# Kernel tuning notes

Measured on AMD Instinct MI355X. Metric: run time of the kernel, lower is better.

## Reference

```python
import jax, jax.numpy as jnp
import numpy as np

D_MODEL = 1024
N_HIDDEN = 64   # per-head dim (outer factor of packed proj dim)
N_HEAD = 16
B, L = 2, 2048


def setup_inputs() -> dict:
    key = jax.random.key(0)
    ks = jax.random.split(key, 7)
    s = 0.02
    return {
        "q": jax.random.normal(ks[0], (B, L, D_MODEL), dtype=jnp.float32),
        "k": jax.random.normal(ks[1], (B, L, D_MODEL), dtype=jnp.float32),
        "v": jax.random.normal(ks[2], (B, L, D_MODEL), dtype=jnp.float32),
        # torch nn.Linear weights: shape (out_features, in_features), y = x @ W.T
        "W_Q": jax.random.normal(ks[3], (N_HIDDEN * N_HEAD, D_MODEL), dtype=jnp.float32) * s,
        "W_K": jax.random.normal(ks[4], (N_HIDDEN * N_HEAD, D_MODEL), dtype=jnp.float32) * s,
        "W_V": jax.random.normal(ks[5], (N_HIDDEN * N_HEAD, D_MODEL), dtype=jnp.float32) * s,
        "W_O": jax.random.normal(ks[6], (D_MODEL, N_HEAD * N_HIDDEN), dtype=jnp.float32) * s,
    }


def reference(q, k, v, W_Q, W_K, W_V, W_O):
    b, l, _ = q.shape
    # projections (bias=False)
    qp = q @ W_Q.T  # [b,l,n_hidden*n_head]
    kp = k @ W_K.T
    vp = v @ W_V.T
    # rearrange 'b l (c h) -> b l c h' with c=n_hidden: hidden is OUTER factor
    qh = qp.reshape(b, l, N_HIDDEN, N_HEAD)
    kh = kp.reshape(b, l, N_HIDDEN, N_HEAD)
    vh = vp.reshape(b, l, N_HIDDEN, N_HEAD)
    scores = jnp.einsum('bldh,bjdh->bhlj', qh, kh) / np.float32(np.sqrt(N_HIDDEN))
    attn = jax.nn.softmax(scores, axis=-1)
    out = jnp.einsum('bhlj,bjdh->bldh', attn, vh)  # [b,l,n_hidden,n_head]
    out = out.reshape(b, l, N_HIDDEN * N_HEAD)      # 'b l d h -> b l (d h)'
    return out @ W_O.T
```

## Files before the change

### kernel.cpp

```cpp
#include <hip/hip_runtime.h>
#include <hip/hip_bf16.h>
#include <stdint.h>

typedef __attribute__((ext_vector_type(8))) short short8;
typedef __attribute__((ext_vector_type(4))) float f32x4;
typedef __attribute__((ext_vector_type(16))) float f32x16;
typedef __attribute__((ext_vector_type(2))) int int2v;
typedef unsigned short u16;
typedef unsigned int u32;


__device__ __forceinline__ u16 bf16rne(float f) {
  u32 u = __builtin_bit_cast(u32, f);
  u += 0x7FFFu + ((u >> 16) & 1u);
  return (u16)(u >> 16);
}

__device__ __forceinline__ u32 cvtpk(float lo, float hi) {
  u32 r;
  asm("v_cvt_pk_bf16_f32 %0, %1, %2" : "=v"(r) : "v"(lo), "v"(hi));
  return r;
}

__device__ __forceinline__ void gl_lds16(const u16* g, u16* l) {
  __builtin_amdgcn_global_load_lds((const __attribute__((address_space(1))) void*)g,
                                   (__attribute__((address_space(3))) void*)l, 16, 0, 0);
}

struct CastArgs {
  const float* src[7];
  u16* dst[7];
  int n4[7];
};

__global__ void cast_all(CastArgs a) {
  const int id = blockIdx.y;
  const float* __restrict__ s = a.src[id];
  u16* __restrict__ d = a.dst[id];
  const int stride = gridDim.x * blockDim.x;
  const int i0 = blockIdx.x * blockDim.x + threadIdx.x;
  if (id < 6) {
    const int n4 = a.n4[id];
    for (int i = i0; i < n4; i += stride) {
      float4 v = ((const float4*)s)[i];
      u32 lo = (u32)bf16rne(v.x) | ((u32)bf16rne(v.y) << 16);
      u32 hi = (u32)bf16rne(v.z) | ((u32)bf16rne(v.w) << 16);
      ((uint2*)d)[i] = make_uint2(lo, hi);
    }
  } else {
    const int n = a.n4[6];
    for (int i = i0; i < n; i += stride) {
      int row = i >> 10, c = i & 1023;
      int hh = c >> 6, dd = c & 63;
      d[i] = bf16rne(s[(row << 10) + dd * 16 + hh]);
    }
  }
}

template<int AHEADS>
__device__ __forceinline__ void gemm_body(const u16* __restrict__ A, const u16* __restrict__ Bw,
                                          void* __restrict__ Cd, int epi, float ascale) {
  const int bn = blockIdx.x * 128, bm = blockIdx.y * 128;
  const int tid = threadIdx.x, lane = tid & 63, w = tid >> 6;
  const int wr = w >> 1, wc = w & 1;
  __shared__ __align__(16) u16 As[128 * 64];
  __shared__ __align__(16) u16 Bs[128 * 64];
  f32x4 acc[4][4];
#pragma unroll
  for (int m = 0; m < 4; ++m)
#pragma unroll
    for (int n = 0; n < 4; ++n) acc[m][n] = (f32x4){0.f, 0.f, 0.f, 0.f};

  for (int kt = 0; kt < 16; ++kt) {
#pragma unroll
    for (int i = 0; i < 4; ++i) {
      int c = tid + i * 256;
      int row = c >> 3, kc = c & 7;
      int swz = (kc ^ (row & 7)) << 3;
      const u16* srcA;
      if (AHEADS) {
        int bA = bm >> 11;
        int lrow = (bm & 2047) + row;
        srcA = A + ((size_t)(bA * 16 + kt) * 2048 + lrow) * 64 + swz;
      } else {
        srcA = A + (size_t)(bm + row) * 1024 + kt * 64 + swz;
      }
      gl_lds16(srcA, &As[c * 8]);
      const u16* srcB = Bw + (size_t)(bn + row) * 1024 + kt * 64 + swz;
      gl_lds16(srcB, &Bs[c * 8]);
    }
    __syncthreads();
#pragma unroll
    for (int ks = 0; ks < 2; ++ks) {
      const int ck = ks * 4 + (lane >> 4);
      short8 af[4], bfr[4];
#pragma unroll
      for (int m = 0; m < 4; ++m) {
        int r = wr * 64 + m * 16 + (lane & 15);
        af[m] = *(const short8*)&As[(r * 8 + (ck ^ (r & 7))) * 8];
      }
#pragma unroll
      for (int n = 0; n < 4; ++n) {
        int r = wc * 64 + n * 16 + (lane & 15);
        bfr[n] = *(const short8*)&Bs[(r * 8 + (ck ^ (r & 7))) * 8];
      }
#pragma unroll
      for (int m = 0; m < 4; ++m)
#pragma unroll
        for (int n = 0; n < 4; ++n)
          acc[m][n] = __builtin_amdgcn_mfma_f32_16x16x32_bf16(af[m], bfr[n], acc[m][n], 0, 0, 0);
    }
    __syncthreads();
  }

  const int lrow4 = (lane >> 4) << 2;
  const int h = lane & 15;
  if (epi == 0) {
    u16* D = (u16*)Cd;
    const int dbase = (bn + wc * 64) >> 4;
#pragma unroll
    for (int m = 0; m < 4; ++m)
#pragma unroll
      for (int i = 0; i < 4; ++i) {
        int R = bm + wr * 64 + m * 16 + lrow4 + i;
        int b = R >> 11, l = R & 2047;
        u32 lo = (u32)bf16rne(acc[m][0][i] * ascale) | ((u32)bf16rne(acc[m][1][i] * ascale) << 16);
        u32 hi = (u32)bf16rne(acc[m][2][i] * ascale) | ((u32)bf16rne(acc[m][3][i] * ascale) << 16);
        size_t addr = ((size_t)((b * 16 + h) * 2048 + l)) * 64 + dbase;
        *(uint2*)(D + addr) = make_uint2(lo, hi);
      }
  } else if (epi == 1) {
    u16* D = (u16*)Cd;
    const int dbase = (bn + wc * 64) >> 4;
    const int b = bm >> 11;
#pragma unroll
    for (int m = 0; m < 4; ++m) {
      int l0 = (bm & 2047) + wr * 64 + m * 16 + lrow4;
#pragma unroll
      for (int n = 0; n < 4; ++n) {
        int d = dbase + n;
        u32 lo = (u32)bf16rne(acc[m][n][0]) | ((u32)bf16rne(acc[m][n][1]) << 16);
        u32 hi = (u32)bf16rne(acc[m][n][2]) | ((u32)bf16rne(acc[m][n][3]) << 16);
        size_t addr = ((size_t)((b * 16 + h) * 64 + d)) * 2048 + l0;
        *(uint2*)(D + addr) = make_uint2(lo, hi);
      }
    }
  } else {
    float* D = (float*)Cd;
#pragma unroll
    for (int m = 0; m < 4; ++m)
#pragma unroll
      for (int i = 0; i < 4; ++i) {
        int R = bm + wr * 64 + m * 16 + lrow4 + i;
        size_t base = (size_t)R * 1024 + bn + wc * 64 + (lane & 15);
#pragma unroll
        for (int n = 0; n < 4; ++n) D[base + n * 16] = acc[m][n][i];
      }
  }
}

struct ProjArgs { const u16* A[3]; const u16* W[3]; u16* D[3]; float scale[3]; };

__global__ __launch_bounds__(256, 2) void gemm_proj(ProjArgs pa) {
  const int z = blockIdx.z;
  gemm_body<0>(pa.A[z], pa.W[z], pa.D[z], z == 2 ? 1 : 0, pa.scale[z]);
}

__global__ __launch_bounds__(256, 2) void gemm_oproj(const u16* __restrict__ A,
                                                     const u16* __restrict__ W,
                                                     float* __restrict__ C) {
  gemm_body<1>(A, W, C, 2, 1.0f);
}

__global__ __launch_bounds__(128, 2) void attn_kernel(const u16* __restrict__ Qh,
                                                      const u16* __restrict__ Kh,
                                                      const u16* __restrict__ Vt,
                                                      u16* __restrict__ Oh) {
  const int hb = blockIdx.x;
  const int qt = blockIdx.y;
  const int tid = threadIdx.x, lane = tid & 63, w = tid >> 6;
  const int l31 = lane & 31, hi = lane >> 5;
  __shared__ __align__(16) u16 Ks[2][64 * 64];
  __shared__ __align__(16) u16 Vs[2][64 * 64];

  const u16* Qg = Qh + (size_t)hb * (2048 * 64);
  const u16* Kg = Kh + (size_t)hb * (2048 * 64);
  const u16* Vg = Vt + (size_t)hb * (64 * 2048);
  const int qrow = qt * 64 + w * 32 + l31;

  short8 qf[4];
#pragma unroll
  for (int ks = 0; ks < 4; ++ks)
    qf[ks] = *(const short8*)(Qg + (size_t)qrow * 64 + ks * 16 + hi * 8);

  int rs[4], sw[4];
#pragma unroll
  for (int i = 0; i < 4; ++i) {
    int c = tid + i * 128;
    rs[i] = c >> 3;
    sw[i] = (((c & 7) ^ (rs[i] & 7)) << 3);
  }

#pragma unroll
  for (int i = 0; i < 4; ++i) {
    int c = tid + i * 128;
    gl_lds16(Kg + (size_t)rs[i] * 64 + sw[i], &Ks[0][c * 8]);
    gl_lds16(Vg + (size_t)rs[i] * 2048 + sw[i], &Vs[0][c * 8]);
  }
  __syncthreads();

  f32x16 oacc0 = {}, oacc1 = {};
  float lrow = 0.f;

  int buf = 0;
  for (int t = 0; t < 32; ++t) {
    if (t < 31) {
      const size_t ko = (size_t)(t + 1) * (64 * 64);
      const int vo = (t + 1) * 64;
#pragma unroll
      for (int i = 0; i < 4; ++i) {
        int c = tid + i * 128;
        gl_lds16(Kg + ko + (size_t)rs[i] * 64 + sw[i], &Ks[buf ^ 1][c * 8]);
        gl_lds16(Vg + (size_t)rs[i] * 2048 + vo + sw[i], &Vs[buf ^ 1][c * 8]);
      }
    }

    f32x16 s0 = {}, s1 = {};
    __builtin_amdgcn_s_setprio(1);
#pragma unroll
    for (int ks = 0; ks < 4; ++ks) {
      const int ck = 2 * ks + hi;
      const int r0 = l31, r1 = 32 + l31;
      short8 k0 = *(const short8*)&Ks[buf][(r0 * 8 + (ck ^ (r0 & 7))) * 8];
      short8 k1 = *(const short8*)&Ks[buf][(r1 * 8 + (ck ^ (r1 & 7))) * 8];
      s0 = __builtin_amdgcn_mfma_f32_32x32x16_bf16(k0, qf[ks], s0, 0, 0, 0);
      s1 = __builtin_amdgcn_mfma_f32_32x32x16_bf16(k1, qf[ks], s1, 0, 0, 0);
    }
    __builtin_amdgcn_s_setprio(0);

#pragma unroll
    for (int i = 0; i < 16; ++i) {
      s0[i] = __builtin_amdgcn_exp2f(s0[i]);
      s1[i] = __builtin_amdgcn_exp2f(s1[i]);
    }
    {
      f32x16 a01 = s0 + s1;
      float r8[8];
#pragma unroll
      for (int i = 0; i < 8; ++i) r8[i] = a01[i] + a01[i + 8];
#pragma unroll
      for (int i = 0; i < 4; ++i) r8[i] += r8[i + 4];
      float rsum = (r8[0] + r8[1]) + (r8[2] + r8[3]);
      int2v pr = __builtin_amdgcn_permlane32_swap(__builtin_bit_cast(int, rsum),
                                                  __builtin_bit_cast(int, rsum), false, false);
      lrow += __builtin_bit_cast(float, pr[0]) + __builtin_bit_cast(float, pr[1]);
    }

#pragma unroll
    for (int c = 0; c < 4; ++c) {
      float pe0, pe1, pe2, pe3, pe4, pe5, pe6, pe7;
      if (c < 2) {
        const int s8 = (c & 1) * 8;
        pe0 = s0[s8 + 0]; pe1 = s0[s8 + 1]; pe2 = s0[s8 + 2]; pe3 = s0[s8 + 3];
        pe4 = s0[s8 + 4]; pe5 = s0[s8 + 5]; pe6 = s0[s8 + 6]; pe7 = s0[s8 + 7];
      } else {
        const int s8 = (c & 1) * 8;
        pe0 = s1[s8 + 0]; pe1 = s1[s8 + 1]; pe2 = s1[s8 + 2]; pe3 = s1[s8 + 3];
        pe4 = s1[s8 + 4]; pe5 = s1[s8 + 5]; pe6 = s1[s8 + 6]; pe7 = s1[s8 + 7];
      }
      u32 a0 = cvtpk(pe0, pe1), a1 = cvtpk(pe2, pe3);
      u32 a2 = cvtpk(pe4, pe5), a3 = cvtpk(pe6, pe7);
      int2v w02 = __builtin_amdgcn_permlane32_swap((int)a0, (int)a2, false, false);
      int2v w13 = __builtin_amdgcn_permlane32_swap((int)a1, (int)a3, false, false);
      union { u32 wu[4]; short8 v; } un;
      un.wu[0] = (u32)w02[0]; un.wu[1] = (u32)w13[0];
      un.wu[2] = (u32)w02[1]; un.wu[3] = (u32)w13[1];
      const int ckv = 2 * c + hi;
      const int rv0 = l31, rv1 = 32 + l31;
      short8 v0 = *(const short8*)&Vs[buf][(rv0 * 8 + (ckv ^ (rv0 & 7))) * 8];
      short8 v1 = *(const short8*)&Vs[buf][(rv1 * 8 + (ckv ^ (rv1 & 7))) * 8];
      __builtin_amdgcn_s_setprio(1);
      oacc0 = __builtin_amdgcn_mfma_f32_32x32x16_bf16(v0, un.v, oacc0, 0, 0, 0);
      oacc1 = __builtin_amdgcn_mfma_f32_32x32x16_bf16(v1, un.v, oacc1, 0, 0, 0);
      __builtin_amdgcn_s_setprio(0);
    }
    __syncthreads();
    buf ^= 1;
  }

  const float inv = 1.0f / lrow;
  u16* Og = Oh + (size_t)hb * (2048 * 64) + (size_t)qrow * 64;
#pragma unroll
  for (int dblk = 0; dblk < 2; ++dblk) {
#pragma unroll
    for (int r = 0; r < 16; r += 2) {
      const int d = dblk * 32 + (r & 3) + 8 * (r >> 2) + 4 * hi;
      float v0 = (dblk ? oacc1[r] : oacc0[r]) * inv;
      float v1 = (dblk ? oacc1[r + 1] : oacc0[r + 1]) * inv;
      *(u32*)(Og + d) = (u32)bf16rne(v0) | ((u32)bf16rne(v1) << 16);
    }
  }
}

extern "C" void kernel_launch(void* const* d_in, const int* in_sizes, int n_in,
                              void* d_out, int out_size, void* d_ws, size_t ws_size,
                              hipStream_t stream) {
  const float* q = (const float*)d_in[0];
  const float* k = (const float*)d_in[1];
  const float* v = (const float*)d_in[2];
  const float* WQ = (const float*)d_in[3];
  const float* WK = (const float*)d_in[4];
  const float* WV = (const float*)d_in[5];
  const float* WO = (const float*)d_in[6];
  float* out = (float*)d_out;
  char* ws = (char*)d_ws;
  const size_t MB = 1024 * 1024;
  if (ws_size < 64 * MB) return;

  u16* qb  = (u16*)(ws + 0 * MB);
  u16* kb  = (u16*)(ws + 8 * MB);
  u16* vb  = (u16*)(ws + 16 * MB);
  u16* WQb = (u16*)(ws + 24 * MB);
  u16* WKb = (u16*)(ws + 26 * MB);
  u16* WVb = (u16*)(ws + 28 * MB);
  u16* WOt = (u16*)(ws + 30 * MB);
  u16* Qh  = (u16*)(ws + 32 * MB);
  u16* Kh  = (u16*)(ws + 40 * MB);
  u16* Vt  = (u16*)(ws + 48 * MB);
  u16* Ohd = (u16*)(ws + 56 * MB);

  CastArgs ca;
  ca.src[0] = q;  ca.dst[0] = qb;  ca.n4[0] = (4096 * 1024) / 4;
  ca.src[1] = k;  ca.dst[1] = kb;  ca.n4[1] = (4096 * 1024) / 4;
  ca.src[2] = v;  ca.dst[2] = vb;  ca.n4[2] = (4096 * 1024) / 4;
  ca.src[3] = WQ; ca.dst[3] = WQb; ca.n4[3] = (1024 * 1024) / 4;
  ca.src[4] = WK; ca.dst[4] = WKb; ca.n4[4] = (1024 * 1024) / 4;
  ca.src[5] = WV; ca.dst[5] = WVb; ca.n4[5] = (1024 * 1024) / 4;
  ca.src[6] = WO; ca.dst[6] = WOt; ca.n4[6] = 1024 * 1024;
  cast_all<<<dim3(256, 7), 256, 0, stream>>>(ca);

  ProjArgs pa;
  pa.A[0] = qb; pa.W[0] = WQb; pa.D[0] = Qh;  pa.scale[0] = 0.18033688011f;
  pa.A[1] = kb; pa.W[1] = WKb; pa.D[1] = Kh;  pa.scale[1] = 1.0f;
  pa.A[2] = vb; pa.W[2] = WVb; pa.D[2] = Vt;  pa.scale[2] = 1.0f;
  gemm_proj<<<dim3(8, 32, 3), 256, 0, stream>>>(pa);

  attn_kernel<<<dim3(32, 32), 128, 0, stream>>>(Qh, Kh, Vt, Ohd);

  gemm_oproj<<<dim3(8, 32), 256, 0, stream>>>(Ohd, WOt, out);
}
```

Baseline: 135.9 us.

## Double-buffer GEMM tiles and prefetch two stages ahead with explicit vmcnt waits

Result: no change. 138.4 us (+1.9%).

```diff
diff --git a/kernel.cpp b/kernel.cpp
--- a/kernel.cpp
+++ b/kernel.cpp
@@ -9,6 +9,13 @@
 typedef unsigned short u16;
 typedef unsigned int u32;
 
+
+#define WAIT_VM8() do { asm volatile("s_waitcnt vmcnt(8)" ::: "memory"); \
+                        __builtin_amdgcn_sched_barrier(0); } while (0)
+#define WAIT_VM0() do { asm volatile("s_waitcnt vmcnt(0)" ::: "memory"); \
+                        __builtin_amdgcn_sched_barrier(0); } while (0)
+#define BARRIER()  do { __builtin_amdgcn_s_barrier(); \
+                        __builtin_amdgcn_sched_barrier(0); } while (0)
 
 __device__ __forceinline__ u16 bf16rne(float f) {
   u32 u = __builtin_bit_cast(u32, f);
@@ -63,15 +70,15 @@
   const int bn = blockIdx.x * 128, bm = blockIdx.y * 128;
   const int tid = threadIdx.x, lane = tid & 63, w = tid >> 6;
   const int wr = w >> 1, wc = w & 1;
-  __shared__ __align__(16) u16 As[128 * 64];
-  __shared__ __align__(16) u16 Bs[128 * 64];
+  __shared__ __align__(16) u16 As[2][128 * 64];
+  __shared__ __align__(16) u16 Bs[2][128 * 64];
   f32x4 acc[4][4];
 #pragma unroll
   for (int m = 0; m < 4; ++m)
 #pragma unroll
     for (int n = 0; n < 4; ++n) acc[m][n] = (f32x4){0.f, 0.f, 0.f, 0.f};
 
-  for (int kt = 0; kt < 16; ++kt) {
+  auto STAGE = [&](int kt, int b) {
 #pragma unroll
     for (int i = 0; i < 4; ++i) {
       int c = tid + i * 256;
@@ -85,11 +92,13 @@
       } else {
         srcA = A + (size_t)(bm + row) * 1024 + kt * 64 + swz;
       }
-      gl_lds16(srcA, &As[c * 8]);
+      gl_lds16(srcA, &As[b][c * 8]);
       const u16* srcB = Bw + (size_t)(bn + row) * 1024 + kt * 64 + swz;
-      gl_lds16(srcB, &Bs[c * 8]);
-    }
-    __syncthreads();
+      gl_lds16(srcB, &Bs[b][c * 8]);
+    }
+  };
+
+  auto COMPUTE = [&](int b) {
 #pragma unroll
     for (int ks = 0; ks < 2; ++ks) {
       const int ck = ks * 4 + (lane >> 4);
@@ -97,12 +106,12 @@
 #pragma unroll
       for (int m = 0; m < 4; ++m) {
         int r = wr * 64 + m * 16 + (lane & 15);
-        af[m] = *(const short8*)&As[(r * 8 + (ck ^ (r & 7))) * 8];
+        af[m] = *(const short8*)&As[b][(r * 8 + (ck ^ (r & 7))) * 8];
       }
 #pragma unroll
       for (int n = 0; n < 4; ++n) {
         int r = wc * 64 + n * 16 + (lane & 15);
-        bfr[n] = *(const short8*)&Bs[(r * 8 + (ck ^ (r & 7))) * 8];
+        bfr[n] = *(const short8*)&Bs[b][(r * 8 + (ck ^ (r & 7))) * 8];
       }
 #pragma unroll
       for (int m = 0; m < 4; ++m)
@@ -110,8 +119,20 @@
         for (int n = 0; n < 4; ++n)
           acc[m][n] = __builtin_amdgcn_mfma_f32_16x16x32_bf16(af[m], bfr[n], acc[m][n], 0, 0, 0);
     }
-    __syncthreads();
-  }
+  };
+
+  STAGE(0, 0);
+  STAGE(1, 1);
+  for (int kt = 0; kt < 15; ++kt) {
+    WAIT_VM8();
+    BARRIER();
+    COMPUTE(kt & 1);
+    BARRIER();
+    if (kt < 14) STAGE(kt + 2, kt & 1);
+  }
+  WAIT_VM0();
+  BARRIER();
+  COMPUTE(1);
 
   const int lrow4 = (lane >> 4) << 2;
   const int h = lane & 15;
@@ -201,38 +222,29 @@
     sw[i] = (((c & 7) ^ (rs[i] & 7)) << 3);
   }
 
-#pragma unroll
-  for (int i = 0; i < 4; ++i) {
-    int c = tid + i * 128;
-    gl_lds16(Kg + (size_t)rs[i] * 64 + sw[i], &Ks[0][c * 8]);
-    gl_lds16(Vg + (size_t)rs[i] * 2048 + sw[i], &Vs[0][c * 8]);
-  }
-  __syncthreads();
+  auto STAGE = [&](int t, int b) {
+    const size_t ko = (size_t)t * (64 * 64);
+    const int vo = t * 64;
+#pragma unroll
+    for (int i = 0; i < 4; ++i) {
+      int c = tid + i * 128;
+      gl_lds16(Kg + ko + (size_t)rs[i] * 64 + sw[i], &Ks[b][c * 8]);
+      gl_lds16(Vg + (size_t)rs[i] * 2048 + vo + sw[i], &Vs[b][c * 8]);
+    }
+  };
 
   f32x16 oacc0 = {}, oacc1 = {};
   float lrow = 0.f;
 
-  int buf = 0;
-  for (int t = 0; t < 32; ++t) {
-    if (t < 31) {
-      const size_t ko = (size_t)(t + 1) * (64 * 64);
-      const int vo = (t + 1) * 64;
-#pragma unroll
-      for (int i = 0; i < 4; ++i) {
-        int c = tid + i * 128;
-        gl_lds16(Kg + ko + (size_t)rs[i] * 64 + sw[i], &Ks[buf ^ 1][c * 8]);
-        gl_lds16(Vg + (size_t)rs[i] * 2048 + vo + sw[i], &Vs[buf ^ 1][c * 8]);
-      }
-    }
-
+  auto COMPUTE = [&](int b) {
     f32x16 s0 = {}, s1 = {};
     __builtin_amdgcn_s_setprio(1);
 #pragma unroll
     for (int ks = 0; ks < 4; ++ks) {
       const int ck = 2 * ks + hi;
       const int r0 = l31, r1 = 32 + l31;
-      short8 k0 = *(const short8*)&Ks[buf][(r0 * 8 + (ck ^ (r0 & 7))) * 8];
-      short8 k1 = *(const short8*)&Ks[buf][(r1 * 8 + (ck ^ (r1 & 7))) * 8];
+      short8 k0 = *(const short8*)&Ks[b][(r0 * 8 + (ck ^ (r0 & 7))) * 8];
+      short8 k1 = *(const short8*)&Ks[b][(r1 * 8 + (ck ^ (r1 & 7))) * 8];
       s0 = __builtin_amdgcn_mfma_f32_32x32x16_bf16(k0, qf[ks], s0, 0, 0, 0);
       s1 = __builtin_amdgcn_mfma_f32_32x32x16_bf16(k1, qf[ks], s1, 0, 0, 0);
     }
@@ -277,16 +289,27 @@
       un.wu[2] = (u32)w02[1]; un.wu[3] = (u32)w13[1];
       const int ckv = 2 * c + hi;
       const int rv0 = l31, rv1 = 32 + l31;
-      short8 v0 = *(const short8*)&Vs[buf][(rv0 * 8 + (ckv ^ (rv0 & 7))) * 8];
-      short8 v1 = *(const short8*)&Vs[buf][(rv1 * 8 + (ckv ^ (rv1 & 7))) * 8];
+      short8 v0 = *(const short8*)&Vs[b][(rv0 * 8 + (ckv ^ (rv0 & 7))) * 8];
+      short8 v1 = *(const short8*)&Vs[b][(rv1 * 8 + (ckv ^ (rv1 & 7))) * 8];
       __builtin_amdgcn_s_setprio(1);
       oacc0 = __builtin_amdgcn_mfma_f32_32x32x16_bf16(v0, un.v, oacc0, 0, 0, 0);
       oacc1 = __builtin_amdgcn_mfma_f32_32x32x16_bf16(v1, un.v, oacc1, 0, 0, 0);
       __builtin_amdgcn_s_setprio(0);
     }
-    __syncthreads();
-    buf ^= 1;
-  }
+  };
+
+  STAGE(0, 0);
+  STAGE(1, 1);
+  for (int t = 0; t < 31; ++t) {
+    WAIT_VM8();
+    BARRIER();
+    COMPUTE(t & 1);
+    BARRIER();
+    if (t < 30) STAGE(t + 2, t & 1);
+  }
+  WAIT_VM0();
+  BARRIER();
+  COMPUTE(1);
 
   const float inv = 1.0f / lrow;
   u16* Og = Oh + (size_t)hb * (2048 * 64) + (size_t)qrow * 64;
```
